# Kernel tuning notes

Hardware: AMD Instinct MI355X
Metric: run time of the kernel (lower is better)

The kernel has to match this reference:

```python
import jax, jax.numpy as jnp
import numpy as np

HEAD_SIZE = 16
HIDDEN = 1024
NEG_INF = -1e9


def setup_inputs() -> dict:
    key = jax.random.key(0)
    ks = jax.random.split(key, 9)
    B, S, H = 2, 2048, HIDDEN
    q = jax.random.normal(ks[0], (B, S, H), dtype=jnp.float32)
    k = jax.random.normal(ks[1], (B, S, H), dtype=jnp.float32)
    v = jax.random.normal(ks[2], (B, S, H), dtype=jnp.float32)
    mask = jnp.ones((B, S), dtype=jnp.int32)
    scale = 1.0 / np.sqrt(H)
    wq = jax.random.normal(ks[3], (H, H), dtype=jnp.float32) * scale
    bq = jnp.zeros((H,), dtype=jnp.float32)
    wk = jax.random.normal(ks[4], (H, H), dtype=jnp.float32) * scale
    bk = jnp.zeros((H,), dtype=jnp.float32)
    wv = jax.random.normal(ks[5], (H, H), dtype=jnp.float32) * scale
    bv = jnp.zeros((H,), dtype=jnp.float32)
    return {"q": q, "k": k, "v": v, "mask": mask,
            "wq": wq, "bq": bq, "wk": wk, "bk": bk, "wv": wv, "bv": bv}


def _split_heads(x):
    # [B, S, H] -> [B, n_heads, S, head_dim]
    B, S, H = x.shape
    return x.reshape(B, S, HEAD_SIZE, H // HEAD_SIZE).transpose(0, 2, 1, 3)


def reference(q, k, v, mask, wq, bq, wk, bk, wv, bv):
    B, S, H = q.shape
    qh = _split_heads(q @ wq + bq)  # [B, nH, S, d]
    kh = _split_heads(k @ wk + bk)
    vh = _split_heads(v @ wv + bv)
    # scores scaled by sqrt(hidden_size) -- faithful to original (not head_dim)
    scores = jnp.einsum('bhqd,bhkd->bhqk', qh, kh) / jnp.sqrt(jnp.float32(H))
    # original: mask[0] of shape [B,S] -> [B,1,S,1], masks query rows
    m = mask.astype(jnp.float32)[:, None, :, None]  # [B,1,S,1]
    scores = scores + NEG_INF * (1.0 - m)
    weights = jax.nn.softmax(scores, axis=-1)
    out = jnp.einsum('bhqk,bhkd->bhqd', weights, vh)  # [B, nH, S, d]
    return out.transpose(0, 2, 1, 3).reshape(B, S, H)
```

## Files before the change

kernel.cpp:

```cpp
#include <hip/hip_runtime.h>
#include <hip/hip_bf16.h>
#include <math.h>

typedef __bf16 bf16_t;
typedef __bf16 bf16x8 __attribute__((ext_vector_type(8)));
typedef __bf16 bf16x4 __attribute__((ext_vector_type(4)));
typedef float floatx4 __attribute__((ext_vector_type(4)));
typedef float floatx16 __attribute__((ext_vector_type(16)));
typedef unsigned int u32;
typedef u32 u32x4 __attribute__((ext_vector_type(4)));

#define QSCALE 0.045084222f

__device__ __forceinline__ void gload_lds16(const bf16_t* g, bf16_t* l) {
  __builtin_amdgcn_global_load_lds(
      (const __attribute__((address_space(1))) void*)(g),
      (__attribute__((address_space(3))) void*)(l), 16, 0, 0);
}

__device__ __forceinline__ float fast_exp2(float x) {
  float r;
  asm("v_exp_f32 %0, %1" : "=v"(r) : "v"(x));
  return r;
}

__device__ __forceinline__ u32 cvt_pk_bf16(float lo, float hi) {
  u32 r;
  asm("v_cvt_pk_bf16_f32 %0, %1, %2" : "=v"(r) : "v"(lo), "v"(hi));
  return r;
}

__device__ __forceinline__ floatx16 zero16() {
  floatx16 z;
#pragma unroll
  for (int i = 0; i < 16; ++i) z[i] = 0.0f;
  return z;
}

__global__ __launch_bounds__(256) void prep_k(
    const float* __restrict__ q, const float* __restrict__ k,
    const float* __restrict__ v, const float* __restrict__ wq,
    const float* __restrict__ wk, const float* __restrict__ wv,
    bf16_t* __restrict__ xb, bf16_t* __restrict__ wt) {
  const int z = blockIdx.y;
  const int t = threadIdx.x;
  if (blockIdx.x < 2048) {
    const float* src = (z == 0) ? q : (z == 1) ? k : v;
    bf16_t* dst = xb + (size_t)z * 4194304u;
    const int i = (blockIdx.x * 256 + t) * 8;
    float4 f0 = *(const float4*)(src + i);
    float4 f1 = *(const float4*)(src + i + 4);
    bf16x8 hv;
    hv[0] = (bf16_t)f0.x; hv[1] = (bf16_t)f0.y;
    hv[2] = (bf16_t)f0.z; hv[3] = (bf16_t)f0.w;
    hv[4] = (bf16_t)f1.x; hv[5] = (bf16_t)f1.y;
    hv[6] = (bf16_t)f1.z; hv[7] = (bf16_t)f1.w;
    *(bf16x8*)(dst + i) = hv;
  } else {
    __shared__ float tile[32][33];
    const int bi = blockIdx.x - 2048;
    const int bx = bi & 31, by = bi >> 5;
    const float* src = (z == 0) ? wq : (z == 1) ? wk : wv;
    bf16_t* dst = wt + (size_t)z * 1048576u;
    const int tx = t & 31, ty = t >> 5;
    const int x = bx * 32 + tx, y = by * 32 + ty;
#pragma unroll
    for (int i = 0; i < 32; i += 8)
      tile[ty + i][tx] = src[(size_t)(y + i) * 1024 + x];
    __syncthreads();
    const int x2 = by * 32 + tx, y2 = bx * 32 + ty;
#pragma unroll
    for (int i = 0; i < 32; i += 8)
      dst[(size_t)(y2 + i) * 1024 + x2] = (bf16_t)tile[tx][ty + i];
  }
}

__global__ __launch_bounds__(256, 2) void qkv_gemm_k(
    const bf16_t* __restrict__ xb3, const bf16_t* __restrict__ wt3,
    const float* __restrict__ bq, const float* __restrict__ bk,
    const float* __restrict__ bv, bf16_t* __restrict__ Qh,
    bf16_t* __restrict__ Kh, bf16_t* __restrict__ Vt) {
  const int proj = blockIdx.z;
  const bf16_t* X = xb3 + (size_t)proj * 4194304u;
  const bf16_t* Wt = wt3 + (size_t)proj * 1048576u;
  const float* bias = (proj == 0) ? bq : (proj == 1) ? bk : bv;

  __shared__ __align__(16) bf16_t As[2][128 * 64];
  __shared__ __align__(16) bf16_t Bs[2][128 * 64];

  const int t = threadIdx.x;
  const int lane = t & 63;
  const int w = t >> 6;
  const int wm = (w >> 1) * 64;
  const int wn = (w & 1) * 64;
  const int m0 = blockIdx.x * 128;
  const int n0 = blockIdx.y * 128;
  const int lm = lane & 15;
  const int lq = lane >> 4;

  int srow[4], sg[4];
#pragma unroll
  for (int c = 0; c < 4; ++c) {
    const int E = c * 2048 + t * 8;
    srow[c] = E >> 6;
    sg[c] = (((E >> 3) & 7) ^ (srow[c] & 7)) * 8;
  }

  floatx4 acc[4][4];
#pragma unroll
  for (int i = 0; i < 4; ++i)
#pragma unroll
    for (int j = 0; j < 4; ++j) acc[i][j] = (floatx4){0.f, 0.f, 0.f, 0.f};

#define GSTAGE(k0, buf)                                                       \
  {                                                                           \
    _Pragma("unroll") for (int c = 0; c < 4; ++c) {                           \
      const int E = c * 2048 + t * 8;                                         \
      gload_lds16(X + (size_t)(m0 + srow[c]) * 1024 + (k0) + sg[c],           \
                  As[buf] + E);                                               \
      gload_lds16(Wt + (size_t)(n0 + srow[c]) * 1024 + (k0) + sg[c],          \
                  Bs[buf] + E);                                               \
    }                                                                         \
  }

  GSTAGE(0, 0);
  __syncthreads();

  int cur = 0;
  for (int k0 = 0; k0 < 1024; k0 += 64) {
    if (k0 < 960) GSTAGE(k0 + 64, cur ^ 1);

#pragma unroll
    for (int kc = 0; kc < 2; ++kc) {
      bf16x8 a[4], b[4];
#pragma unroll
      for (int i = 0; i < 4; ++i) {
        const int ch = ((kc * 4 + lq) ^ (lm & 7)) * 8;
        a[i] = *(const bf16x8*)(As[cur] + (wm + i * 16 + lm) * 64 + ch);
        b[i] = *(const bf16x8*)(Bs[cur] + (wn + i * 16 + lm) * 64 + ch);
      }
      if (proj < 2) {
#pragma unroll
        for (int i = 0; i < 4; ++i)
#pragma unroll
          for (int j = 0; j < 4; ++j)
            acc[i][j] = __builtin_amdgcn_mfma_f32_16x16x32_bf16(b[j], a[i],
                                                               acc[i][j], 0, 0, 0);
      } else {
#pragma unroll
        for (int i = 0; i < 4; ++i)
#pragma unroll
          for (int j = 0; j < 4; ++j)
            acc[i][j] = __builtin_amdgcn_mfma_f32_16x16x32_bf16(a[i], b[j],
                                                               acc[i][j], 0, 0, 0);
      }
    }

    __syncthreads();
    cur ^= 1;
  }
#undef GSTAGE

  if (proj == 2) {
#pragma unroll
    for (int j = 0; j < 4; ++j) {
      const int gn = n0 + wn + j * 16 + lm;
      const float bval = bias[gn];
      const int h = gn >> 6, d = gn & 63;
#pragma unroll
      for (int i = 0; i < 4; ++i) {
        const int gm = m0 + wm + i * 16 + lq * 4;
        const int bb = gm >> 11, s0 = gm & 2047;
        bf16x4 pk;
#pragma unroll
        for (int ii = 0; ii < 4; ++ii) pk[ii] = (bf16_t)(acc[i][j][ii] + bval);
        *(bf16x4*)(Vt + (((size_t)bb * 16 + h) * 64 + d) * 2048 + s0) = pk;
      }
    }
  } else {
    bf16_t* outp = (proj == 0) ? Qh : Kh;
    const float scale = (proj == 0) ? QSCALE : 1.0f;
#pragma unroll
    for (int j = 0; j < 4; ++j) {
      const int nb = n0 + wn + j * 16 + lq * 4;
      float bs4[4];
#pragma unroll
      for (int ii = 0; ii < 4; ++ii) bs4[ii] = bias[nb + ii];
      const int h = nb >> 6, d0 = nb & 63;
#pragma unroll
      for (int i = 0; i < 4; ++i) {
        const int gm = m0 + wm + i * 16 + lm;
        const int bb = gm >> 11, s = gm & 2047;
        bf16x4 pk;
#pragma unroll
        for (int ii = 0; ii < 4; ++ii)
          pk[ii] = (bf16_t)((acc[i][j][ii] + bs4[ii]) * scale);
        *(bf16x4*)(outp + (((size_t)bb * 16 + h) * 2048 + s) * 64 + d0) = pk;
      }
    }
  }
}

__global__ __launch_bounds__(512, 2) void attn_k(
    const bf16_t* __restrict__ Qh, const bf16_t* __restrict__ Kh,
    const bf16_t* __restrict__ Vt, float* __restrict__ out) {
  __shared__ __align__(16) unsigned char smem[67584];
  bf16_t* KsB = (bf16_t*)smem;
  bf16_t* VsB = (bf16_t*)(smem + 32768);
  float4* Xo = (float4*)smem;
  float* Xl = (float*)(smem + 65536);

  const int t = threadIdx.x;
  const int lane = t & 63;
  const int w = t >> 6;
  const int grp = w >> 2;
  const int wq4 = w & 3;
  const int tg = t & 255;
  const int lc = lane & 31;
  const int hi = lane >> 5;
  const int koff = grp * 1024;
  const int b = blockIdx.x >> 4, h = blockIdx.x & 15;
  const int q0 = blockIdx.y * 256;
  const size_t bh = (size_t)b * 16 + h;
  const bf16_t* Qb = Qh + bh * (2048 * 64);
  const bf16_t* Kb = Kh + bh * (2048 * 64);
  const bf16_t* Vb = Vt + bh * (64 * 2048);

  bf16x8 qf[2][4];
#pragma unroll
  for (int qg = 0; qg < 2; ++qg)
#pragma unroll
    for (int kk = 0; kk < 4; ++kk)
      qf[qg][kk] = *(const bf16x8*)(Qb +
          (size_t)(q0 + wq4 * 64 + qg * 32 + lc) * 64 + kk * 16 + hi * 8);

  bf16x8 ones;
#pragma unroll
  for (int j = 0; j < 8; ++j) ones[j] = (bf16_t)1.0f;

  floatx16 accO[2][2], accL[2];
#pragma unroll
  for (int qg = 0; qg < 2; ++qg) {
    accO[qg][0] = zero16();
    accO[qg][1] = zero16();
    accL[qg] = zero16();
  }

#define STAGE(kt, buf)                                                        \
  {                                                                           \
    _Pragma("unroll") for (int cc = 0; cc < 2; ++cc) {                        \
      const int e = cc * 2048 + tg * 8;                                       \
      const int r = e >> 6, gk = ((e >> 3) & 7) ^ (r & 7);                    \
      gload_lds16(Kb + (size_t)(koff + (kt) + r) * 64 + gk * 8,               \
                  KsB + (grp * 2 + (buf)) * 4096 + e);                        \
      gload_lds16(Vb + (size_t)r * 2048 + koff + (kt) + gk * 8,               \
                  VsB + (grp * 2 + (buf)) * 4096 + e);                        \
    }                                                                         \
  }

  STAGE(0, 0);
  __syncthreads();

  int cur = 0;
  for (int it = 0; it < 16; ++it) {
    if (it + 1 < 16) STAGE((it + 1) * 64, cur ^ 1);

    const bf16_t* Kc = KsB + (grp * 2 + cur) * 4096;
    const bf16_t* Vc = VsB + (grp * 2 + cur) * 4096;

    floatx16 accS[2][2];
    __builtin_amdgcn_s_setprio(1);
#pragma unroll
    for (int jn = 0; jn < 2; ++jn) {
      const int krow = jn * 32 + lc;
      floatx16 z0 = zero16(), z1 = zero16();
#pragma unroll
      for (int kk = 0; kk < 4; ++kk) {
        const bf16x8 kf = *(const bf16x8*)(Kc + krow * 64 +
                                           ((kk * 2 + hi) ^ (krow & 7)) * 8);
        z0 = __builtin_amdgcn_mfma_f32_32x32x16_bf16(kf, qf[0][kk], z0, 0, 0, 0);
        z1 = __builtin_amdgcn_mfma_f32_32x32x16_bf16(kf, qf[1][kk], z1, 0, 0, 0);
      }
      accS[0][jn] = z0;
      accS[1][jn] = z1;
    }
    __builtin_amdgcn_s_setprio(0);

    bf16x8 pf[2][4];
#pragma unroll
    for (int qg = 0; qg < 2; ++qg)
#pragma unroll
      for (int jn = 0; jn < 2; ++jn) {
        u32 pk8[8];
#pragma unroll
        for (int p = 0; p < 8; ++p)
          pk8[p] = cvt_pk_bf16(fast_exp2(accS[qg][jn][2 * p]),
                               fast_exp2(accS[qg][jn][2 * p + 1]));
        asm volatile("v_permlane32_swap_b32 %0, %1" : "+v"(pk8[0]), "+v"(pk8[2]));
        asm volatile("v_permlane32_swap_b32 %0, %1" : "+v"(pk8[1]), "+v"(pk8[3]));
        asm volatile("v_permlane32_swap_b32 %0, %1" : "+v"(pk8[4]), "+v"(pk8[6]));
        asm volatile("v_permlane32_swap_b32 %0, %1" : "+v"(pk8[5]), "+v"(pk8[7]));
        u32x4 f0 = {pk8[0], pk8[1], pk8[2], pk8[3]};
        u32x4 f1 = {pk8[4], pk8[5], pk8[6], pk8[7]};
        pf[qg][jn * 2] = __builtin_bit_cast(bf16x8, f0);
        pf[qg][jn * 2 + 1] = __builtin_bit_cast(bf16x8, f1);
      }

    __builtin_amdgcn_s_setprio(1);
#pragma unroll
    for (int ks = 0; ks < 4; ++ks) {
#pragma unroll
      for (int jd = 0; jd < 2; ++jd) {
        const int vrow = jd * 32 + lc;
        const bf16x8 vf = *(const bf16x8*)(Vc + vrow * 64 +
                                           ((ks * 2 + hi) ^ (vrow & 7)) * 8);
        accO[0][jd] =
            __builtin_amdgcn_mfma_f32_32x32x16_bf16(vf, pf[0][ks], accO[0][jd], 0, 0, 0);
        accO[1][jd] =
            __builtin_amdgcn_mfma_f32_32x32x16_bf16(vf, pf[1][ks], accO[1][jd], 0, 0, 0);
      }
      accL[0] = __builtin_amdgcn_mfma_f32_32x32x16_bf16(ones, pf[0][ks], accL[0], 0, 0, 0);
      accL[1] = __builtin_amdgcn_mfma_f32_32x32x16_bf16(ones, pf[1][ks], accL[1], 0, 0, 0);
    }
    __builtin_amdgcn_s_setprio(0);

    __syncthreads();
    cur ^= 1;
  }
#undef STAGE

  const int wid = wq4 * 64 + lane;
  if (grp == 1) {
#pragma unroll
    for (int qg = 0; qg < 2; ++qg) {
#pragma unroll
      for (int jd = 0; jd < 2; ++jd)
#pragma unroll
        for (int g = 0; g < 4; ++g) {
          float4 x;
          x.x = accO[qg][jd][4 * g + 0];
          x.y = accO[qg][jd][4 * g + 1];
          x.z = accO[qg][jd][4 * g + 2];
          x.w = accO[qg][jd][4 * g + 3];
          Xo[(qg * 8 + jd * 4 + g) * 256 + wid] = x;
        }
      Xl[qg * 256 + wid] = accL[qg][0];
    }
  }
  __syncthreads();
  if (grp == 0) {
#pragma unroll
    for (int qg = 0; qg < 2; ++qg) {
      const float inv = 1.0f / (accL[qg][0] + Xl[qg * 256 + wid]);
      const int s = q0 + wq4 * 64 + qg * 32 + lc;
      float* op = out + ((size_t)b * 2048 + s) * 1024 + h * 64;
#pragma unroll
      for (int jd = 0; jd < 2; ++jd)
#pragma unroll
        for (int g = 0; g < 4; ++g) {
          const float4 x = Xo[(qg * 8 + jd * 4 + g) * 256 + wid];
          float4 o;
          o.x = (accO[qg][jd][4 * g + 0] + x.x) * inv;
          o.y = (accO[qg][jd][4 * g + 1] + x.y) * inv;
          o.z = (accO[qg][jd][4 * g + 2] + x.z) * inv;
          o.w = (accO[qg][jd][4 * g + 3] + x.w) * inv;
          *(float4*)(op + jd * 32 + g * 8 + hi * 4) = o;
        }
    }
  }
}

extern "C" void kernel_launch(void* const* d_in, const int* in_sizes, int n_in,
                              void* d_out, int out_size, void* d_ws, size_t ws_size,
                              hipStream_t stream) {
  (void)in_sizes; (void)n_in; (void)out_size; (void)ws_size;
  const float* q = (const float*)d_in[0];
  const float* k = (const float*)d_in[1];
  const float* v = (const float*)d_in[2];
  const float* wq = (const float*)d_in[4];
  const float* bq = (const float*)d_in[5];
  const float* wk = (const float*)d_in[6];
  const float* bk = (const float*)d_in[7];
  const float* wv = (const float*)d_in[8];
  const float* bv = (const float*)d_in[9];
  float* out = (float*)d_out;

  bf16_t* ws = (bf16_t*)d_ws;
  bf16_t* Xb = ws;
  bf16_t* Wt = ws + 12582912u;
  bf16_t* Qh = Wt + 3145728u;
  bf16_t* Kh = Qh + 4194304u;
  bf16_t* Vt = Kh + 4194304u;

  prep_k<<<dim3(3072, 3, 1), dim3(256, 1, 1), 0, stream>>>(
      q, k, v, wq, wk, wv, Xb, Wt);
  qkv_gemm_k<<<dim3(32, 8, 3), dim3(256, 1, 1), 0, stream>>>(
      Xb, Wt, bq, bk, bv, Qh, Kh, Vt);
  attn_k<<<dim3(32, 8, 1), dim3(512, 1, 1), 0, stream>>>(Qh, Kh, Vt, out);
}
```

Before: 187.8 us.

## Fuse fp32-to-bf16 activation conversion into QKV GEMM and shrink N tile

```diff
diff --git a/kernel.cpp b/kernel.cpp
--- a/kernel.cpp
+++ b/kernel.cpp
@@ -38,132 +38,147 @@
 }
 
 __global__ __launch_bounds__(256) void prep_k(
-    const float* __restrict__ q, const float* __restrict__ k,
-    const float* __restrict__ v, const float* __restrict__ wq,
-    const float* __restrict__ wk, const float* __restrict__ wv,
-    bf16_t* __restrict__ xb, bf16_t* __restrict__ wt) {
+    const float* __restrict__ wq, const float* __restrict__ wk,
+    const float* __restrict__ wv, bf16_t* __restrict__ wt) {
   const int z = blockIdx.y;
   const int t = threadIdx.x;
-  if (blockIdx.x < 2048) {
-    const float* src = (z == 0) ? q : (z == 1) ? k : v;
-    bf16_t* dst = xb + (size_t)z * 4194304u;
-    const int i = (blockIdx.x * 256 + t) * 8;
-    float4 f0 = *(const float4*)(src + i);
-    float4 f1 = *(const float4*)(src + i + 4);
-    bf16x8 hv;
-    hv[0] = (bf16_t)f0.x; hv[1] = (bf16_t)f0.y;
-    hv[2] = (bf16_t)f0.z; hv[3] = (bf16_t)f0.w;
-    hv[4] = (bf16_t)f1.x; hv[5] = (bf16_t)f1.y;
-    hv[6] = (bf16_t)f1.z; hv[7] = (bf16_t)f1.w;
-    *(bf16x8*)(dst + i) = hv;
-  } else {
-    __shared__ float tile[32][33];
-    const int bi = blockIdx.x - 2048;
-    const int bx = bi & 31, by = bi >> 5;
-    const float* src = (z == 0) ? wq : (z == 1) ? wk : wv;
-    bf16_t* dst = wt + (size_t)z * 1048576u;
-    const int tx = t & 31, ty = t >> 5;
-    const int x = bx * 32 + tx, y = by * 32 + ty;
-#pragma unroll
-    for (int i = 0; i < 32; i += 8)
-      tile[ty + i][tx] = src[(size_t)(y + i) * 1024 + x];
-    __syncthreads();
-    const int x2 = by * 32 + tx, y2 = bx * 32 + ty;
-#pragma unroll
-    for (int i = 0; i < 32; i += 8)
-      dst[(size_t)(y2 + i) * 1024 + x2] = (bf16_t)tile[tx][ty + i];
-  }
-}
-
-__global__ __launch_bounds__(256, 2) void qkv_gemm_k(
-    const bf16_t* __restrict__ xb3, const bf16_t* __restrict__ wt3,
+  __shared__ float tile[32][33];
+  const int bi = blockIdx.x;
+  const int bx = bi & 31, by = bi >> 5;
+  const float* src = (z == 0) ? wq : (z == 1) ? wk : wv;
+  bf16_t* dst = wt + (size_t)z * 1048576u;
+  const int tx = t & 31, ty = t >> 5;
+  const int x = bx * 32 + tx, y = by * 32 + ty;
+#pragma unroll
+  for (int i = 0; i < 32; i += 8)
+    tile[ty + i][tx] = src[(size_t)(y + i) * 1024 + x];
+  __syncthreads();
+  const int x2 = by * 32 + tx, y2 = bx * 32 + ty;
+#pragma unroll
+  for (int i = 0; i < 32; i += 8)
+    dst[(size_t)(y2 + i) * 1024 + x2] = (bf16_t)tile[tx][ty + i];
+}
+
+__global__ __launch_bounds__(256, 3) void qkv_gemm_k(
+    const float* __restrict__ q, const float* __restrict__ k,
+    const float* __restrict__ v, const bf16_t* __restrict__ wt3,
     const float* __restrict__ bq, const float* __restrict__ bk,
     const float* __restrict__ bv, bf16_t* __restrict__ Qh,
     bf16_t* __restrict__ Kh, bf16_t* __restrict__ Vt) {
   const int proj = blockIdx.z;
-  const bf16_t* X = xb3 + (size_t)proj * 4194304u;
+  const float* X = (proj == 0) ? q : (proj == 1) ? k : v;
   const bf16_t* Wt = wt3 + (size_t)proj * 1048576u;
   const float* bias = (proj == 0) ? bq : (proj == 1) ? bk : bv;
 
   __shared__ __align__(16) bf16_t As[2][128 * 64];
-  __shared__ __align__(16) bf16_t Bs[2][128 * 64];
+  __shared__ __align__(16) bf16_t Bs[2][64 * 64];
 
   const int t = threadIdx.x;
   const int lane = t & 63;
   const int w = t >> 6;
   const int wm = (w >> 1) * 64;
-  const int wn = (w & 1) * 64;
+  const int wn = (w & 1) * 32;
   const int m0 = blockIdx.x * 128;
-  const int n0 = blockIdx.y * 128;
+  const int n0 = blockIdx.y * 64;
   const int lm = lane & 15;
   const int lq = lane >> 4;
 
-  int srow[4], sg[4];
-#pragma unroll
-  for (int c = 0; c < 4; ++c) {
-    const int E = c * 2048 + t * 8;
-    srow[c] = E >> 6;
-    sg[c] = (((E >> 3) & 7) ^ (srow[c] & 7)) * 8;
-  }
-
-  floatx4 acc[4][4];
+  floatx4 acc[4][2];
 #pragma unroll
   for (int i = 0; i < 4; ++i)
 #pragma unroll
-    for (int j = 0; j < 4; ++j) acc[i][j] = (floatx4){0.f, 0.f, 0.f, 0.f};
-
-#define GSTAGE(k0, buf)                                                       \
+    for (int j = 0; j < 2; ++j) acc[i][j] = (floatx4){0.f, 0.f, 0.f, 0.f};
+
+  float4 av[4][2];
+
+#define A_LOAD(k0)                                                            \
   {                                                                           \
     _Pragma("unroll") for (int c = 0; c < 4; ++c) {                           \
       const int E = c * 2048 + t * 8;                                         \
-      gload_lds16(X + (size_t)(m0 + srow[c]) * 1024 + (k0) + sg[c],           \
-                  As[buf] + E);                                               \
-      gload_lds16(Wt + (size_t)(n0 + srow[c]) * 1024 + (k0) + sg[c],          \
+      const int r = E >> 6, gk = ((E >> 3) & 7) ^ (r & 7);                    \
+      const float* gp = X + (size_t)(m0 + r) * 1024 + (k0) + gk * 8;          \
+      av[c][0] = *(const float4*)gp;                                          \
+      av[c][1] = *(const float4*)(gp + 4);                                    \
+    }                                                                         \
+  }
+
+#define A_STORE(buf)                                                          \
+  {                                                                           \
+    _Pragma("unroll") for (int c = 0; c < 4; ++c) {                           \
+      const int E = c * 2048 + t * 8;                                         \
+      bf16x8 hv;                                                              \
+      hv[0] = (bf16_t)av[c][0].x; hv[1] = (bf16_t)av[c][0].y;                 \
+      hv[2] = (bf16_t)av[c][0].z; hv[3] = (bf16_t)av[c][0].w;                 \
+      hv[4] = (bf16_t)av[c][1].x; hv[5] = (bf16_t)av[c][1].y;                 \
+      hv[6] = (bf16_t)av[c][1].z; hv[7] = (bf16_t)av[c][1].w;                 \
+      *(bf16x8*)(As[buf] + E) = hv;                                           \
+    }                                                                         \
+  }
+
+#define B_STAGE(k0, buf)                                                      \
+  {                                                                           \
+    _Pragma("unroll") for (int c = 0; c < 2; ++c) {                           \
+      const int E = c * 2048 + t * 8;                                         \
+      const int r = E >> 6, gk = ((E >> 3) & 7) ^ (r & 7);                    \
+      gload_lds16(Wt + (size_t)(n0 + r) * 1024 + (k0) + gk * 8,               \
                   Bs[buf] + E);                                               \
     }                                                                         \
   }
 
-  GSTAGE(0, 0);
+  A_LOAD(0);
+  A_STORE(0);
+  B_STAGE(0, 0);
   __syncthreads();
 
   int cur = 0;
   for (int k0 = 0; k0 < 1024; k0 += 64) {
-    if (k0 < 960) GSTAGE(k0 + 64, cur ^ 1);
+    if (k0 < 960) {
+      A_LOAD(k0 + 64);
+      B_STAGE(k0 + 64, cur ^ 1);
+    }
 
 #pragma unroll
     for (int kc = 0; kc < 2; ++kc) {
-      bf16x8 a[4], b[4];
+      bf16x8 a[4], b[2];
 #pragma unroll
       for (int i = 0; i < 4; ++i) {
         const int ch = ((kc * 4 + lq) ^ (lm & 7)) * 8;
         a[i] = *(const bf16x8*)(As[cur] + (wm + i * 16 + lm) * 64 + ch);
-        b[i] = *(const bf16x8*)(Bs[cur] + (wn + i * 16 + lm) * 64 + ch);
+      }
+#pragma unroll
+      for (int j = 0; j < 2; ++j) {
+        const int ch = ((kc * 4 + lq) ^ (lm & 7)) * 8;
+        b[j] = *(const bf16x8*)(Bs[cur] + (wn + j * 16 + lm) * 64 + ch);
       }
       if (proj < 2) {
 #pragma unroll
         for (int i = 0; i < 4; ++i)
 #pragma unroll
-          for (int j = 0; j < 4; ++j)
+          for (int j = 0; j < 2; ++j)
             acc[i][j] = __builtin_amdgcn_mfma_f32_16x16x32_bf16(b[j], a[i],
                                                                acc[i][j], 0, 0, 0);
       } else {
 #pragma unroll
         for (int i = 0; i < 4; ++i)
 #pragma unroll
-          for (int j = 0; j < 4; ++j)
+          for (int j = 0; j < 2; ++j)
             acc[i][j] = __builtin_amdgcn_mfma_f32_16x16x32_bf16(a[i], b[j],
                                                                acc[i][j], 0, 0, 0);
       }
     }
 
+    if (k0 < 960) A_STORE(cur ^ 1);
+
     __syncthreads();
     cur ^= 1;
   }
-#undef GSTAGE
+#undef A_LOAD
+#undef A_STORE
+#undef B_STAGE
 
   if (proj == 2) {
 #pragma unroll
-    for (int j = 0; j < 4; ++j) {
+    for (int j = 0; j < 2; ++j) {
       const int gn = n0 + wn + j * 16 + lm;
       const float bval = bias[gn];
       const int h = gn >> 6, d = gn & 63;
@@ -181,7 +196,7 @@
     bf16_t* outp = (proj == 0) ? Qh : Kh;
     const float scale = (proj == 0) ? QSCALE : 1.0f;
 #pragma unroll
-    for (int j = 0; j < 4; ++j) {
+    for (int j = 0; j < 2; ++j) {
       const int nb = n0 + wn + j * 16 + lq * 4;
       float bs4[4];
 #pragma unroll
@@ -386,15 +401,13 @@
   float* out = (float*)d_out;
 
   bf16_t* ws = (bf16_t*)d_ws;
-  bf16_t* Xb = ws;
-  bf16_t* Wt = ws + 12582912u;
+  bf16_t* Wt = ws;
   bf16_t* Qh = Wt + 3145728u;
   bf16_t* Kh = Qh + 4194304u;
   bf16_t* Vt = Kh + 4194304u;
 
-  prep_k<<<dim3(3072, 3, 1), dim3(256, 1, 1), 0, stream>>>(
-      q, k, v, wq, wk, wv, Xb, Wt);
-  qkv_gemm_k<<<dim3(32, 8, 3), dim3(256, 1, 1), 0, stream>>>(
-      Xb, Wt, bq, bk, bv, Qh, Kh, Vt);
+  prep_k<<<dim3(1024, 3, 1), dim3(256, 1, 1), 0, stream>>>(wq, wk, wv, Wt);
+  qkv_gemm_k<<<dim3(32, 16, 3), dim3(256, 1, 1), 0, stream>>>(
+      q, k, v, Wt, bq, bk, bv, Qh, Kh, Vt);
   attn_k<<<dim3(32, 8, 1), dim3(512, 1, 1), 0, stream>>>(Qh, Kh, Vt, out);
 }
```

After: 202.4 us. 1.08x slower.
